# Performance work log

Hardware: AMD Instinct MI355X
Metric: run time of the kernel (lower is better)

The kernel has to match this reference:

```python
import jax, jax.numpy as jnp
import numpy as np

EPSILON = 0.1
ALPHA = 0.5
N_ITER = 10
N_USERS = 100000


def setup_inputs() -> dict:
    key = jax.random.key(0)
    k1, k2, k3, k4, k5, k6 = jax.random.split(key, 6)
    B, C, F = 2048, 1024, 128
    users = jax.random.randint(k1, (B,), 0, N_USERS)
    items = jax.random.randint(k2, (B, C), 0, C)
    D = jax.random.uniform(k3, (B, C), minval=0.1, maxval=1.0)
    capacities = jax.random.uniform(k4, (C,), minval=0.5, maxval=1.5)
    # ScaledEmbedding: normal init scaled down by embedding_dim
    item_emb = jax.random.normal(k5, (C, F), dtype=jnp.float32) / F
    user_emb = jax.random.normal(k6, (N_USERS, F), dtype=jnp.float32) / F
    return dict(users=users, items=items, D=D, capacities=capacities,
                item_emb=item_emb, user_emb=user_emb)


def reference(users, items, D, capacities, item_emb, user_emb):
    B, C = D.shape
    ie = item_emb[items]            # [B, C, F] gathered candidate embeddings
    ue = user_emb[users]            # [B, F]
    dot = jnp.einsum('bcf,bf->bc', ie, ue)          # batched dot products
    affinity = (1.0 - ALPHA) * dot - ALPHA * (D / jnp.mean(D))
    K = jnp.exp(affinity / EPSILON)                 # [B, C]

    scaling = B / N_USERS
    a = jnp.ones((B,), K.dtype)
    b = capacities * scaling                        # [C]

    def step(carry, _):
        _, v = carry
        u = a / (K @ v)                             # [B]
        v_new = b / (K.T @ u)                       # [C]
        return (u, v_new), None

    (u, v), _ = jax.lax.scan(step, (a, jnp.ones((C,), K.dtype)),
                             None, length=N_ITER)
    P = K * (u[:, None] * v[None, :])               # K * outer(u, v)
    return P
```

## Files before the change

### kernel.cpp

```cpp
#include <hip/hip_runtime.h>
#include <hip/hip_fp16.h>

#define BB      2048
#define CC      1024
#define FF      128
#define NBLK    256
#define RPB     8
#define TPB     512
#define NITER   10
#define SUBR    8
#define SCALING_F (2048.0f / 100000.0f)

__device__ unsigned g_bar;
__device__ float g_meanPart[NBLK];
__device__ float g_colsum[NITER * SUBR * CC];

__device__ __forceinline__ void grid_barrier(int tid) {
    __syncthreads();
    if (tid == 0) {
        unsigned c = __hip_atomic_fetch_add(&g_bar, 1u, __ATOMIC_RELAXED,
                                            __HIP_MEMORY_SCOPE_AGENT);
        unsigned target = (c / NBLK) * NBLK + NBLK;
        while ((int)(__hip_atomic_load(&g_bar, __ATOMIC_RELAXED,
                                       __HIP_MEMORY_SCOPE_AGENT) - target) < 0)
            ;
    }
    __syncthreads();
}

__global__ void __launch_bounds__(TPB)
fused_sinkhorn(const int* __restrict__ users, const int* __restrict__ items,
               const float* __restrict__ D, const float* __restrict__ caps,
               const float* __restrict__ iemb, const float* __restrict__ uemb,
               float* __restrict__ out) {
    const int bid = blockIdx.x, tid = threadIdx.x;
    const int r0 = bid * RPB;

    __shared__ union { float ue[RPB][FF]; float v[CC]; } uv;
    __shared__ __half dott[RPB][CC];
    __shared__ float  Kt[RPB][CC];
    __shared__ float  ush[RPB];
    __shared__ float  red[TPB / 64];
    __shared__ float  s2sh;

    for (int i = bid * TPB + tid; i < NITER * SUBR * CC; i += NBLK * TPB)
        __hip_atomic_store(&g_colsum[i], 0.0f, __ATOMIC_RELAXED,
                           __HIP_MEMORY_SCOPE_AGENT);

    if (tid < 256) {
        int r = tid >> 5, f4 = tid & 31;
        int u = users[r0 + r];
        ((float4*)uv.ue[r])[f4] = ((const float4*)(uemb + (size_t)u * FF))[f4];
    }

    const float4* Dg  = (const float4*)(D + ((size_t)r0 << 10));
    float4*       KtL = (float4*)Kt;
    float p = 0.0f;
    for (int i = tid; i < RPB * CC / 4; i += TPB) {
        float4 d = Dg[i];
        KtL[i] = d;
        p += d.x + d.y + d.z + d.w;
    }
    #pragma unroll
    for (int off = 32; off > 0; off >>= 1) p += __shfl_down(p, off, 64);
    if ((tid & 63) == 0) red[tid >> 6] = p;
    __syncthreads();
    if (tid == 0) {
        float s = 0.0f;
        #pragma unroll
        for (int k = 0; k < TPB / 64; ++k) s += red[k];
        __hip_atomic_store(&g_meanPart[bid], s, __ATOMIC_RELAXED,
                           __HIP_MEMORY_SCOPE_AGENT);
    }

    const float4* us = (const float4*)uv.ue;
    #pragma unroll
    for (int jj = 0; jj < CC / TPB; ++jj) {
        int j = jj * TPB + tid;
        float acc[RPB] = {};
        const float4* ip = (const float4*)(iemb + (size_t)j * FF);
        for (int f4 = 0; f4 < FF / 4; ++f4) {
            float4 a = ip[f4];
            #pragma unroll
            for (int r = 0; r < RPB; ++r) {
                float4 b = us[r * (FF / 4) + f4];
                acc[r] += a.x * b.x + a.y * b.y + a.z * b.z + a.w * b.w;
            }
        }
        #pragma unroll
        for (int r = 0; r < RPB; ++r) dott[r][j] = __float2half(acc[r]);
    }

    grid_barrier(tid);

    if (tid < 64) {
        float s = 0.0f;
        #pragma unroll
        for (int k = 0; k < NBLK / 64; ++k)
            s += __hip_atomic_load(&g_meanPart[tid + 64 * k], __ATOMIC_RELAXED,
                                   __HIP_MEMORY_SCOPE_AGENT);
        #pragma unroll
        for (int off = 32; off > 0; off >>= 1) s += __shfl_down(s, off, 64);
        if (tid == 0) s2sh = 5.0f * (float)(BB * CC) / s;
    }
    __syncthreads();
    const float s2 = s2sh;
    const int4* it4 = (const int4*)(items + ((size_t)r0 << 10));
    for (int i = tid; i < RPB * CC / 4; i += TPB) {
        int4   iv = it4[i];
        float4 d  = KtL[i];
        int    r  = i >> 8;
        float4 kv;
        kv.x = __expf(5.0f * __half2float(dott[r][iv.x]) - s2 * d.x);
        kv.y = __expf(5.0f * __half2float(dott[r][iv.y]) - s2 * d.y);
        kv.z = __expf(5.0f * __half2float(dott[r][iv.z]) - s2 * d.z);
        kv.w = __expf(5.0f * __half2float(dott[r][iv.w]) - s2 * d.w);
        KtL[i] = kv;
    }

    for (int t = 0; t < NITER; ++t) {
        if (t == 0) {
            for (int c = tid; c < CC; c += TPB) uv.v[c] = 1.0f;
        } else {
            float* base = g_colsum + (size_t)(t - 1) * SUBR * CC;
            for (int c = tid; c < CC; c += TPB) {
                float s = 0.0f;
                #pragma unroll
                for (int k = 0; k < SUBR; ++k)
                    s += __hip_atomic_load(&base[k * CC + c], __ATOMIC_RELAXED,
                                           __HIP_MEMORY_SCOPE_AGENT);
                uv.v[c] = caps[c] * SCALING_F / s;
            }
        }
        __syncthreads();

        {
            int r = tid >> 6, l = tid & 63;
            const float4* kr = (const float4*)Kt[r];
            const float4* v4 = (const float4*)uv.v;
            float pp = 0.0f;
            #pragma unroll
            for (int i2 = 0; i2 < 4; ++i2) {
                float4 k = kr[l + i2 * 64], v = v4[l + i2 * 64];
                pp += k.x * v.x + k.y * v.y + k.z * v.z + k.w * v.w;
            }
            #pragma unroll
            for (int off = 32; off > 0; off >>= 1) pp += __shfl_down(pp, off, 64);
            if (l == 0) ush[r] = 1.0f / pp;
        }
        __syncthreads();

        float* cb = g_colsum + ((size_t)t * SUBR + (bid & (SUBR - 1))) * CC;
        for (int c = tid; c < CC; c += TPB) {
            float s = 0.0f;
            #pragma unroll
            for (int r = 0; r < RPB; ++r) s += Kt[r][c] * ush[r];
            atomicAdd(&cb[c], s);
        }

        grid_barrier(tid);
    }

    {
        float* base = g_colsum + (size_t)(NITER - 1) * SUBR * CC;
        for (int c = tid; c < CC; c += TPB) {
            float s = 0.0f;
            #pragma unroll
            for (int k = 0; k < SUBR; ++k)
                s += __hip_atomic_load(&base[k * CC + c], __ATOMIC_RELAXED,
                                       __HIP_MEMORY_SCOPE_AGENT);
            uv.v[c] = caps[c] * SCALING_F / s;
        }
    }
    __syncthreads();

    float4* o4 = (float4*)(out + ((size_t)r0 << 10));
    for (int i = tid; i < RPB * CC / 4; i += TPB) {
        int    r  = i >> 8;
        float4 k  = KtL[i];
        float  ur = ush[r];
        float4 v  = *(const float4*)&uv.v[(i * 4) & (CC - 1)];
        float4 pv;
        pv.x = k.x * ur * v.x;  pv.y = k.y * ur * v.y;
        pv.z = k.z * ur * v.z;  pv.w = k.w * ur * v.w;
        o4[i] = pv;
    }
}

extern "C" void kernel_launch(void* const* d_in, const int* in_sizes, int n_in,
                              void* d_out, int out_size, void* d_ws, size_t ws_size,
                              hipStream_t stream) {
    const int*   users = (const int*)d_in[0];
    const int*   items = (const int*)d_in[1];
    const float* D     = (const float*)d_in[2];
    const float* caps  = (const float*)d_in[3];
    const float* iemb  = (const float*)d_in[4];
    const float* uemb  = (const float*)d_in[5];
    float* out = (float*)d_out;

    hipLaunchKernelGGL(fused_sinkhorn, dim3(NBLK), dim3(TPB), 0, stream,
                       users, items, D, caps, iemb, uemb, out);
}
```

Baseline: 190.9 us.

## Distribute per-iteration column reduction across blocks and publish v via flags

New measurement: 447.8 us. 135% more time.

```diff
diff --git a/kernel.cpp b/kernel.cpp
--- a/kernel.cpp
+++ b/kernel.cpp
@@ -8,12 +8,21 @@
 #define RPB     8
 #define TPB     512
 #define NITER   10
-#define SUBR    8
+#define SUBR    32
 #define SCALING_F (2048.0f / 100000.0f)
 
 __device__ unsigned g_bar;
-__device__ float g_meanPart[NBLK];
-__device__ float g_colsum[NITER * SUBR * CC];
+__device__ unsigned g_done[NITER];
+__device__ float    g_meanPart[NBLK];
+__device__ float    g_colsum[NITER][CC * SUBR];
+__device__ float    g_v[NITER + 1][CC];
+
+__device__ __forceinline__ float atomLoadF(const float* p) {
+    return __hip_atomic_load(p, __ATOMIC_RELAXED, __HIP_MEMORY_SCOPE_AGENT);
+}
+__device__ __forceinline__ void atomStoreF(float* p, float v) {
+    __hip_atomic_store(p, v, __ATOMIC_RELAXED, __HIP_MEMORY_SCOPE_AGENT);
+}
 
 __device__ __forceinline__ void grid_barrier(int tid) {
     __syncthreads();
@@ -44,8 +53,16 @@
     __shared__ float  s2sh;
 
     for (int i = bid * TPB + tid; i < NITER * SUBR * CC; i += NBLK * TPB)
-        __hip_atomic_store(&g_colsum[i], 0.0f, __ATOMIC_RELAXED,
-                           __HIP_MEMORY_SCOPE_AGENT);
+        atomStoreF(&g_colsum[0][0] + i, 0.0f);
+    for (int i = bid * TPB + tid; i < (NITER + 1) * CC; i += NBLK * TPB)
+        atomStoreF(&g_v[0][0] + i, 0.0f);
+
+    float bcap = 0.0f;
+    int   myc  = 0;
+    if (tid < 128) {
+        myc  = (bid << 2) + (tid >> 5);
+        bcap = caps[myc] * SCALING_F;
+    }
 
     if (tid < 256) {
         int r = tid >> 5, f4 = tid & 31;
@@ -69,8 +86,7 @@
         float s = 0.0f;
         #pragma unroll
         for (int k = 0; k < TPB / 64; ++k) s += red[k];
-        __hip_atomic_store(&g_meanPart[bid], s, __ATOMIC_RELAXED,
-                           __HIP_MEMORY_SCOPE_AGENT);
+        atomStoreF(&g_meanPart[bid], s);
     }
 
     const float4* us = (const float4*)uv.ue;
@@ -97,8 +113,7 @@
         float s = 0.0f;
         #pragma unroll
         for (int k = 0; k < NBLK / 64; ++k)
-            s += __hip_atomic_load(&g_meanPart[tid + 64 * k], __ATOMIC_RELAXED,
-                                   __HIP_MEMORY_SCOPE_AGENT);
+            s += atomLoadF(&g_meanPart[tid + 64 * k]);
         #pragma unroll
         for (int off = 32; off > 0; off >>= 1) s += __shfl_down(s, off, 64);
         if (tid == 0) s2sh = 5.0f * (float)(BB * CC) / s;
@@ -122,14 +137,10 @@
         if (t == 0) {
             for (int c = tid; c < CC; c += TPB) uv.v[c] = 1.0f;
         } else {
-            float* base = g_colsum + (size_t)(t - 1) * SUBR * CC;
             for (int c = tid; c < CC; c += TPB) {
-                float s = 0.0f;
-                #pragma unroll
-                for (int k = 0; k < SUBR; ++k)
-                    s += __hip_atomic_load(&base[k * CC + c], __ATOMIC_RELAXED,
-                                           __HIP_MEMORY_SCOPE_AGENT);
-                uv.v[c] = caps[c] * SCALING_F / s;
+                float v;
+                do { v = atomLoadF(&g_v[t][c]); } while (v == 0.0f);
+                uv.v[c] = v;
             }
         }
         __syncthreads();
@@ -150,27 +161,40 @@
         }
         __syncthreads();
 
-        float* cb = g_colsum + ((size_t)t * SUBR + (bid & (SUBR - 1))) * CC;
-        for (int c = tid; c < CC; c += TPB) {
-            float s = 0.0f;
-            #pragma unroll
-            for (int r = 0; r < RPB; ++r) s += Kt[r][c] * ush[r];
-            atomicAdd(&cb[c], s);
-        }
-
-        grid_barrier(tid);
-    }
-
-    {
-        float* base = g_colsum + (size_t)(NITER - 1) * SUBR * CC;
-        for (int c = tid; c < CC; c += TPB) {
-            float s = 0.0f;
-            #pragma unroll
-            for (int k = 0; k < SUBR; ++k)
-                s += __hip_atomic_load(&base[k * CC + c], __ATOMIC_RELAXED,
-                                       __HIP_MEMORY_SCOPE_AGENT);
-            uv.v[c] = caps[c] * SCALING_F / s;
-        }
+        {
+            const int slot = bid & (SUBR - 1);
+            for (int c = tid; c < CC; c += TPB) {
+                float s = 0.0f;
+                #pragma unroll
+                for (int r = 0; r < RPB; ++r) s += Kt[r][c] * ush[r];
+                atomicAdd(&g_colsum[t][(c << 5) | slot], s);
+            }
+        }
+        __syncthreads();
+
+        if ((tid & 63) == 0 && tid < 128) {
+            unsigned c = __hip_atomic_fetch_add(&g_done[t], 1u, __ATOMIC_RELAXED,
+                                                __HIP_MEMORY_SCOPE_AGENT);
+            unsigned target = (c / (2 * NBLK)) * (2 * NBLK) + 2 * NBLK;
+            while ((int)(__hip_atomic_load(&g_done[t], __ATOMIC_RELAXED,
+                                           __HIP_MEMORY_SCOPE_AGENT) - target) < 0)
+                __builtin_amdgcn_s_sleep(1);
+        }
+        asm volatile("" ::: "memory");
+        if (tid < 128) {
+            float pp = atomLoadF(&g_colsum[t][(myc << 5) | (tid & 31)]);
+            #pragma unroll
+            for (int off = 16; off > 0; off >>= 1)
+                pp += __shfl_down(pp, off, 32);
+            if ((tid & 31) == 0)
+                atomStoreF(&g_v[t + 1][myc], bcap / pp);
+        }
+    }
+
+    for (int c = tid; c < CC; c += TPB) {
+        float v;
+        do { v = atomLoadF(&g_v[NITER][c]); } while (v == 0.0f);
+        uv.v[c] = v;
     }
     __syncthreads();
 
```
